# Performance work log

Measured on AMD Instinct MI355X. Metric: run time of the kernel, lower is better.

## Reference

```python
import jax, jax.numpy as jnp
import numpy as np

# priors from init_kwargs
PRIOR_PI = 0.5
PRIOR_S1 = 1.0
PRIOR_S2 = 0.0025
LOG_SQRT_2PI = 0.5 * np.log(2.0 * np.pi).astype(np.float32)


def _normal_logprob(x, sigma):
    # Normal(0, sigma).log_prob(x)
    return -0.5 * (x / sigma) ** 2 - jnp.log(sigma) - LOG_SQRT_2PI


def _mixture_logprob_sum(x, pi, sigma1, sigma2):
    # log(pi * N(x;0,s1) + (1-pi) * N(x;0,s2)).sum(), as in the torch code
    p1 = jnp.exp(_normal_logprob(x, sigma1))
    p2 = jnp.exp(_normal_logprob(x, sigma2))
    return jnp.log(pi * p1 + (1.0 - pi) * p2).sum()


def _sample(pi, rho1, rho2, eps, gum):
    # ScaleMixtureGaussian_VarPost.sample(): gumbel-max over (pi, 1-pi)
    sigma1 = jnp.log1p(jnp.exp(rho1))
    sigma2 = jnp.log1p(jnp.exp(rho2))
    x = jnp.stack((pi, 1.0 - pi), axis=-1)          # [..., 2]
    mode = jnp.argmax(x + gum, axis=-1).astype(pi.dtype)  # [...]
    return mode * sigma1 * eps + (1.0 - mode) * sigma2 * eps


def setup_inputs() -> dict:
    key = jax.random.key(0)
    ks = jax.random.split(key, 12)
    OUT, IN, B = 8192, 4096, 128
    f32 = jnp.float32
    u_w = jax.random.uniform(ks[0], (OUT, IN, 2), dtype=f32, minval=1e-6, maxval=1.0 - 1e-6)
    u_b = jax.random.uniform(ks[1], (OUT, 2), dtype=f32, minval=1e-6, maxval=1.0 - 1e-6)
    return {
        "x": jax.random.normal(ks[2], (B, IN), dtype=f32),
        "w_pi": jax.random.uniform(ks[3], (OUT, IN), dtype=f32),
        "w_rho1": 0.1 * jax.random.normal(ks[4], (OUT, IN), dtype=f32),
        "w_rho2": 0.1 * jax.random.normal(ks[5], (OUT, IN), dtype=f32),
        "b_pi": jax.random.uniform(ks[6], (OUT,), dtype=f32),
        "b_rho1": 0.1 * jax.random.normal(ks[7], (OUT,), dtype=f32),
        "b_rho2": 0.1 * jax.random.normal(ks[8], (OUT,), dtype=f32),
        "eps_w": jax.random.normal(ks[9], (OUT, IN), dtype=f32),
        "eps_b": jax.random.normal(ks[10], (OUT,), dtype=f32),
        "gum_w": -jnp.log(-jnp.log(u_w)),  # Gumbel(0,1)
        "gum_b": -jnp.log(-jnp.log(u_b)),
    }


def reference(x, w_pi, w_rho1, w_rho2, b_pi, b_rho1, b_rho2, eps_w, eps_b, gum_w, gum_b):
    weight = _sample(w_pi, w_rho1, w_rho2, eps_w, gum_w)   # [OUT, IN]
    bias = _sample(b_pi, b_rho1, b_rho2, eps_b, gum_b)     # [OUT]

    log_prior = (_mixture_logprob_sum(weight, PRIOR_PI, PRIOR_S1, PRIOR_S2)
                 + _mixture_logprob_sum(bias, PRIOR_PI, PRIOR_S1, PRIOR_S2))

    sig_w1 = jnp.log1p(jnp.exp(w_rho1))
    sig_w2 = jnp.log1p(jnp.exp(w_rho2))
    sig_b1 = jnp.log1p(jnp.exp(b_rho1))
    sig_b2 = jnp.log1p(jnp.exp(b_rho2))
    log_post = (_mixture_logprob_sum(weight, w_pi, sig_w1, sig_w2)
                + _mixture_logprob_sum(bias, b_pi, sig_b1, sig_b2))

    out = x @ weight.T + bias  # F.linear
    return out, log_prior, log_post
```

## Files before the change

### kernel.cpp

```cpp
#include <hip/hip_runtime.h>

#define OUTN 8192
#define INN  4096
#define BN   128

namespace {

typedef __attribute__((ext_vector_type(8))) short bf16x8;
typedef __attribute__((ext_vector_type(4))) float f32x4;

struct alignas(16) f4 { float v[4]; };
struct alignas(8)  h4 { short v[4]; };

constexpr float C_HLOG2PI = 0.91893853f;
constexpr float C_LN2     = 0.69314718f;

__device__ __forceinline__ short f2bf(float f) {
    unsigned u = __float_as_uint(f);
    u += 0x7fffu + ((u >> 16) & 1u);
    return (short)(u >> 16);
}

__device__ __forceinline__ float prior_lp(float w) {
    float lp1 = -0.5f * w * w - C_HLOG2PI;
    float a   = w * 400.0f;
    float lp2 = -0.5f * a * a + 5.0725261f;
    return __logf(0.5f * __expf(lp1) + 0.5f * __expf(lp2));
}
__device__ __forceinline__ float post_lp(float w, float pi_, float s1, float ls1,
                                         float s2, float ls2) {
    float u1  = __fdividef(w, s1);
    float u2  = __fdividef(w, s2);
    float lq1 = -0.5f * u1 * u1 - ls1 - C_HLOG2PI;
    float lq2 = -0.5f * u2 * u2 - ls2 - C_HLOG2PI;
    return __logf(pi_ * __expf(lq1) + (1.0f - pi_) * __expf(lq2));
}
__device__ __forceinline__ float sample_w(float pi_, float rho1, float rho2, float ep,
                                          float g0, float g1,
                                          float& s1, float& ls1, float& s2, float& ls2) {
    s1  = __logf(1.0f + __expf(rho1));
    s2  = __logf(1.0f + __expf(rho2));
    ls1 = __logf(s1);
    ls2 = __logf(s2);
    bool mode1 = ((1.0f - pi_) + g1) > (pi_ + g0);
    return (mode1 ? s1 : s2) * ep;
}

constexpr int OT = 32;
constexpr int KC = 32;
constexpr int NT = 256;
constexpr int KSTR = 40;

__global__ __launch_bounds__(256)
void prep(const float* __restrict__ x, short* __restrict__ xb,
          const float* __restrict__ b_pi, const float* __restrict__ b_rho1,
          const float* __restrict__ b_rho2, const float* __restrict__ eps_b,
          const float* __restrict__ gum_b,
          float* __restrict__ bias_vals, float* __restrict__ bpart)
{
    __shared__ float red[8];
    const int tid = threadIdx.x;
    if (blockIdx.x < 256) {
        const int i = (blockIdx.x * 256 + tid) * 8;
        f4 a = *(const f4*)&x[i];
        f4 b = *(const f4*)&x[i + 4];
        h4 o0, o1;
        #pragma unroll
        for (int j = 0; j < 4; ++j) { o0.v[j] = f2bf(a.v[j]); o1.v[j] = f2bf(b.v[j]); }
        *(h4*)&xb[i]     = o0;
        *(h4*)&xb[i + 4] = o1;
        return;
    }
    const int bb = blockIdx.x - 256;
    const int o = bb * 256 + tid;
    float pi_ = b_pi[o], rho1 = b_rho1[o], rho2 = b_rho2[o], ep = eps_b[o];
    float g0 = gum_b[2*o], g1 = gum_b[2*o + 1];
    float s1, ls1, s2, ls2;
    float w = sample_w(pi_, rho1, rho2, ep, g0, g1, s1, ls1, s2, ls2);
    bias_vals[o] = w;
    float pa = prior_lp(w);
    float qa = post_lp(w, pi_, s1, ls1, s2, ls2);
    #pragma unroll
    for (int off = 32; off; off >>= 1) {
        pa += __shfl_down(pa, off);
        qa += __shfl_down(qa, off);
    }
    const int wave = tid >> 6;
    if ((tid & 63) == 0) { red[wave] = pa; red[4 + wave] = qa; }
    __syncthreads();
    if (tid == 0) {
        bpart[2*bb    ] = red[0] + red[1] + red[2] + red[3];
        bpart[2*bb + 1] = red[4] + red[5] + red[6] + red[7];
    }
}

__global__ __launch_bounds__(NT, 6)
void bayes_main(const short* __restrict__ xb,
                const float* __restrict__ w_pi,
                const float* __restrict__ w_rho1,
                const float* __restrict__ w_rho2,
                const float* __restrict__ eps_w,
                const float* __restrict__ gum_w,
                const float* __restrict__ bias,
                float* __restrict__ out,
                float* __restrict__ pbuf,
                float* __restrict__ partials,
                int NS)
{
    __shared__ alignas(16) short Wt[2][OT][KSTR];
    __shared__ alignas(16) short Xs[2][BN][KSTR];
    __shared__ float red[8];

    const int tid   = threadIdx.x;
    const int split = blockIdx.x >> 8;
    const int tile  = blockIdx.x & 255;
    const int o0    = tile * OT;

    const int baseCh = 128 / NS;
    const int remCh  = 128 % NS;
    const int nch    = baseCh + (split < remCh ? 1 : 0);
    const int ch0    = split * baseCh + (split < remCh ? split : remCh);
    const int k0     = ch0 * KC;

    float* outp = (split == 0) ? out : pbuf + (size_t)(split - 1) * ((size_t)BN * OUTN);

    const int c = tid & 7;
    const int r = tid >> 3;

    const size_t wbase = (size_t)(o0 + r) * INN + k0;
    const f4* pi4 = (const f4*)(w_pi   + wbase) + c;
    const f4* r14 = (const f4*)(w_rho1 + wbase) + c;
    const f4* r24 = (const f4*)(w_rho2 + wbase) + c;
    const f4* ep4 = (const f4*)(eps_w  + wbase) + c;
    const f4* gm4 = (const f4*)(gum_w  + 2 * wbase) + 2 * c;

    const int xrr = tid >> 1;
    const int xcc = (tid & 1) * 16;
    const short* xsrc = xb + (size_t)xrr * INN + k0 + xcc;

    f32x4 acc00 = {0.f,0.f,0.f,0.f}, acc01 = {0.f,0.f,0.f,0.f};
    f32x4 acc10 = {0.f,0.f,0.f,0.f}, acc11 = {0.f,0.f,0.f,0.f};
    float priorAcc = 0.0f, postAcc = 0.0f;

    const int wv_  = tid >> 6;
    const int lane = tid & 63;
    const int lrow = lane & 15;
    const int lgo  = (lane >> 4) * 8;

    f4 vpi = pi4[0], vr1 = r14[0], vr2 = r24[0], vep = ep4[0];
    f4 vga = gm4[0], vgb = gm4[1];
    bf16x8 xv0 = *(const bf16x8*)(xsrc);
    bf16x8 xv1 = *(const bf16x8*)(xsrc + 8);

    #pragma unroll 1
    for (int t = 0; t < nch; ++t) {
        const int p = t & 1;
        h4 wb;
        #pragma unroll
        for (int i = 0; i < 4; ++i) {
            const f4& g = (i < 2) ? vga : vgb;
            float g0 = g.v[(i & 1) * 2], g1 = g.v[(i & 1) * 2 + 1];
            float pi_ = vpi.v[i], ep = vep.v[i];
            float s1  = __logf(1.0f + __expf(vr1.v[i]));
            float s2  = __logf(1.0f + __expf(vr2.v[i]));
            float ls1 = __logf(s1), ls2 = __logf(s2);
            bool  m1  = ((1.0f - pi_) + g1) > (pi_ + g0);
            float sm  = m1 ? s1 : s2;
            float so  = m1 ? s2 : s1;
            float lsm = m1 ? ls1 : ls2;
            float lso = m1 ? ls2 : ls1;
            float wm  = m1 ? pi_ : 1.0f - pi_;
            float w   = sm * ep;
            wb.v[i] = f2bf(w);
            float wsq = w * w;
            float dlp = 5.9914645f - 79999.5f * wsq;
            priorAcc += -0.5f * wsq + __logf(1.0f + __expf(dlp));
            float uo   = __fdividef(w, so);
            float epsq = ep * ep;
            float dlq  = 0.5f * (epsq - uo * uo) + (lsm - lso);
            postAcc += -0.5f * epsq - lsm
                       + __logf(wm + (1.0f - wm) * __expf(dlq));
        }

        const int tn = (t + 1 < nch) ? t + 1 : 0;
        vpi = pi4[8*tn]; vr1 = r14[8*tn]; vr2 = r24[8*tn]; vep = ep4[8*tn];
        vga = gm4[16*tn]; vgb = gm4[16*tn + 1];

        *(h4*)&Wt[p][r][4 * c] = wb;
        *(bf16x8*)&Xs[p][xrr][xcc]     = xv0;
        *(bf16x8*)&Xs[p][xrr][xcc + 8] = xv1;
        xv0 = *(const bf16x8*)(xsrc + 32*tn);
        xv1 = *(const bf16x8*)(xsrc + 32*tn + 8);

        asm volatile("s_waitcnt lgkmcnt(0)" ::: "memory");
        __builtin_amdgcn_s_barrier();
        asm volatile("" ::: "memory");

        bf16x8 a0 = *(const bf16x8*)&Xs[p][32 * wv_      + lrow][lgo];
        bf16x8 a1 = *(const bf16x8*)&Xs[p][32 * wv_ + 16 + lrow][lgo];
        bf16x8 b0 = *(const bf16x8*)&Wt[p][lrow     ][lgo];
        bf16x8 b1 = *(const bf16x8*)&Wt[p][16 + lrow][lgo];
        acc00 = __builtin_amdgcn_mfma_f32_16x16x32_bf16(a0, b0, acc00, 0, 0, 0);
        acc01 = __builtin_amdgcn_mfma_f32_16x16x32_bf16(a0, b1, acc01, 0, 0, 0);
        acc10 = __builtin_amdgcn_mfma_f32_16x16x32_bf16(a1, b0, acc10, 0, 0, 0);
        acc11 = __builtin_amdgcn_mfma_f32_16x16x32_bf16(a1, b1, acc11, 0, 0, 0);
    }

    {
        const float ne = (float)(4 * nch);
        priorAcc -= ne * (C_HLOG2PI + C_LN2);
        postAcc  -= ne * C_HLOG2PI;
    }

    {
        const int oc = o0 + lrow;
        const int bb = 32 * wv_ + (lane >> 4) * 4;
        const float bv0 = bias ? bias[oc]      : 0.0f;
        const float bv1 = bias ? bias[oc + 16] : 0.0f;
        #pragma unroll
        for (int j = 0; j < 4; ++j) {
            outp[(size_t)(bb      + j) * OUTN + oc     ] = acc00[j] + bv0;
            outp[(size_t)(bb      + j) * OUTN + oc + 16] = acc01[j] + bv1;
            outp[(size_t)(bb + 16 + j) * OUTN + oc     ] = acc10[j] + bv0;
            outp[(size_t)(bb + 16 + j) * OUTN + oc + 16] = acc11[j] + bv1;
        }
    }

    #pragma unroll
    for (int off = 32; off; off >>= 1) {
        priorAcc += __shfl_down(priorAcc, off);
        postAcc  += __shfl_down(postAcc, off);
    }
    if ((tid & 63) == 0) { red[wv_] = priorAcc; red[4 + wv_] = postAcc; }
    __syncthreads();
    if (tid == 0) {
        partials[2*blockIdx.x    ] = red[0] + red[1] + red[2] + red[3];
        partials[2*blockIdx.x + 1] = red[4] + red[5] + red[6] + red[7];
    }
}

__global__ __launch_bounds__(256)
void reduce_final(float* __restrict__ out, const float* __restrict__ pbuf,
                  const float* __restrict__ bias, int nsplit,
                  const float* __restrict__ partials, int cnt,
                  float* __restrict__ out_scalars)
{
    const int tid = threadIdx.x;
    const size_t i = ((size_t)blockIdx.x * 256 + tid) * 4;
    const int o = (int)(i & (OUTN - 1));
    f4 a  = *(const f4*)&out[i];
    f4 bq = *(const f4*)&bias[o];
    #pragma unroll 1
    for (int s = 0; s < nsplit - 1; ++s) {
        f4 p = *(const f4*)&pbuf[(size_t)s * ((size_t)BN * OUTN) + i];
        #pragma unroll
        for (int j = 0; j < 4; ++j) a.v[j] += p.v[j];
    }
    #pragma unroll
    for (int j = 0; j < 4; ++j) a.v[j] += bq.v[j];
    *(f4*)&out[i] = a;

    if (blockIdx.x == 0) {
        __shared__ double sp[4], sq[4];
        double p = 0.0, q = 0.0;
        for (int j = tid; j < cnt; j += 256) {
            p += (double)partials[2*j];
            q += (double)partials[2*j + 1];
        }
        #pragma unroll
        for (int off = 32; off; off >>= 1) {
            p += __shfl_down(p, off);
            q += __shfl_down(q, off);
        }
        const int wave = tid >> 6;
        if ((tid & 63) == 0) { sp[wave] = p; sq[wave] = q; }
        __syncthreads();
        if (tid == 0) {
            out_scalars[0] = (float)(sp[0] + sp[1] + sp[2] + sp[3]);
            out_scalars[1] = (float)(sq[0] + sq[1] + sq[2] + sq[3]);
        }
    }
}

__global__ __launch_bounds__(256)
void bayes_final(const float* __restrict__ partials, int cnt,
                 float* __restrict__ out_scalars)
{
    __shared__ double sp[4], sq[4];
    const int tid = threadIdx.x;
    double p = 0.0, q = 0.0;
    for (int j = tid; j < cnt; j += 256) {
        p += (double)partials[2*j];
        q += (double)partials[2*j + 1];
    }
    #pragma unroll
    for (int off = 32; off; off >>= 1) {
        p += __shfl_down(p, off);
        q += __shfl_down(q, off);
    }
    const int wave = tid >> 6;
    if ((tid & 63) == 0) { sp[wave] = p; sq[wave] = q; }
    __syncthreads();
    if (tid == 0) {
        out_scalars[0] = (float)(sp[0] + sp[1] + sp[2] + sp[3]);
        out_scalars[1] = (float)(sq[0] + sq[1] + sq[2] + sq[3]);
    }
}

}

extern "C" void kernel_launch(void* const* d_in, const int* in_sizes, int n_in,
                              void* d_out, int out_size, void* d_ws, size_t ws_size,
                              hipStream_t stream) {
    (void)in_sizes; (void)n_in; (void)out_size;
    const float* x      = (const float*)d_in[0];
    const float* w_pi   = (const float*)d_in[1];
    const float* w_rho1 = (const float*)d_in[2];
    const float* w_rho2 = (const float*)d_in[3];
    const float* b_pi   = (const float*)d_in[4];
    const float* b_rho1 = (const float*)d_in[5];
    const float* b_rho2 = (const float*)d_in[6];
    const float* eps_w  = (const float*)d_in[7];
    const float* eps_b  = (const float*)d_in[8];
    const float* gum_w  = (const float*)d_in[9];
    const float* gum_b  = (const float*)d_in[10];

    float* out = (float*)d_out;
    float* ws  = (float*)d_ws;
    float* bias_vals = ws;
    float* partials  = ws + 8192;
    short* xb        = (short*)(ws + 16384);
    float* pbuf      = ws + 540672;

    const size_t outElems = (size_t)BN * OUTN;
    int NS = 1;
    if      (ws_size >= (540672 + 5 * outElems) * sizeof(float)) NS = 6;
    else if (ws_size >= (540672 + 3 * outElems) * sizeof(float)) NS = 4;
    else if (ws_size >= (540672 + 1 * outElems) * sizeof(float)) NS = 2;

    float* bpart = partials + 2 * 256 * NS;
    const int cnt = 256 * NS + 32;

    prep<<<288, 256, 0, stream>>>(x, xb, b_pi, b_rho1, b_rho2, eps_b, gum_b,
                                  bias_vals, bpart);

    if (NS == 1) {
        bayes_main<<<256, NT, 0, stream>>>(xb, w_pi, w_rho1, w_rho2, eps_w, gum_w,
                                           bias_vals, out, pbuf, partials, 1);
        bayes_final<<<1, 256, 0, stream>>>(partials, cnt, out + outElems);
    } else {
        bayes_main<<<256 * NS, NT, 0, stream>>>(xb, w_pi, w_rho1, w_rho2, eps_w, gum_w,
                                                nullptr, out, pbuf, partials, NS);
        reduce_final<<<(int)(outElems / 4 / 256), 256, 0, stream>>>(
            out, pbuf, bias_vals, NS, partials, cnt, out + outElems);
    }
}
```

Measured before the change: 223.6 us.

## Double K chunk to 64, swizzle X shared tile, single-buffer with two barriers

Raises the per-iteration K chunk from 32 to 64, so each thread samples 8 weights and issues two MFMA k-steps per iteration, halving loop trips and barrier count. The X tile in LDS becomes a single XOR-swizzled buffer to avoid bank conflicts, and the weight tile is single-buffered with syncthreads before and after the stores. Occupancy hint drops from 6 to 5 and split-K count from 6 to 5 to match the larger tile. The trade-off is losing double buffering and the overlap of the next prefetch with LDS writes, plus higher register pressure.

```diff
diff --git a/kernel.cpp b/kernel.cpp
--- a/kernel.cpp
+++ b/kernel.cpp
@@ -47,9 +47,9 @@
 }
 
 constexpr int OT = 32;
-constexpr int KC = 32;
+constexpr int KC = 64;
 constexpr int NT = 256;
-constexpr int KSTR = 40;
+constexpr int WSTR = 72;
 
 __global__ __launch_bounds__(256)
 void prep(const float* __restrict__ x, short* __restrict__ xb,
@@ -94,7 +94,7 @@
     }
 }
 
-__global__ __launch_bounds__(NT, 6)
+__global__ __launch_bounds__(NT, 5)
 void bayes_main(const short* __restrict__ xb,
                 const float* __restrict__ w_pi,
                 const float* __restrict__ w_rho1,
@@ -107,8 +107,8 @@
                 float* __restrict__ partials,
                 int NS)
 {
-    __shared__ alignas(16) short Wt[2][OT][KSTR];
-    __shared__ alignas(16) short Xs[2][BN][KSTR];
+    __shared__ alignas(16) short Wt[OT][WSTR];
+    __shared__ alignas(16) short Xs[BN * KC];
     __shared__ float red[8];
 
     const int tid   = threadIdx.x;
@@ -116,8 +116,8 @@
     const int tile  = blockIdx.x & 255;
     const int o0    = tile * OT;
 
-    const int baseCh = 128 / NS;
-    const int remCh  = 128 % NS;
+    const int baseCh = 64 / NS;
+    const int remCh  = 64 % NS;
     const int nch    = baseCh + (split < remCh ? 1 : 0);
     const int ch0    = split * baseCh + (split < remCh ? split : remCh);
     const int k0     = ch0 * KC;
@@ -128,15 +128,16 @@
     const int r = tid >> 3;
 
     const size_t wbase = (size_t)(o0 + r) * INN + k0;
-    const f4* pi4 = (const f4*)(w_pi   + wbase) + c;
-    const f4* r14 = (const f4*)(w_rho1 + wbase) + c;
-    const f4* r24 = (const f4*)(w_rho2 + wbase) + c;
-    const f4* ep4 = (const f4*)(eps_w  + wbase) + c;
-    const f4* gm4 = (const f4*)(gum_w  + 2 * wbase) + 2 * c;
-
-    const int xrr = tid >> 1;
-    const int xcc = (tid & 1) * 16;
-    const short* xsrc = xb + (size_t)xrr * INN + k0 + xcc;
+    const f4* pi4 = (const f4*)(w_pi   + wbase) + 2 * c;
+    const f4* r14 = (const f4*)(w_rho1 + wbase) + 2 * c;
+    const f4* r24 = (const f4*)(w_rho2 + wbase) + 2 * c;
+    const f4* ep4 = (const f4*)(eps_w  + wbase) + 2 * c;
+    const f4* gm4 = (const f4*)(gum_w + 2 * wbase) + 4 * c;
+
+    const int xr   = tid >> 1;
+    const int xh   = (tid & 1) * 32;
+    const int xswz = (xr & 7) * 8;
+    const short* xsrc = xb + (size_t)xr * INN + k0 + xh;
 
     f32x4 acc00 = {0.f,0.f,0.f,0.f}, acc01 = {0.f,0.f,0.f,0.f};
     f32x4 acc10 = {0.f,0.f,0.f,0.f}, acc11 = {0.f,0.f,0.f,0.f};
@@ -146,32 +147,41 @@
     const int lane = tid & 63;
     const int lrow = lane & 15;
     const int lgo  = (lane >> 4) * 8;
-
-    f4 vpi = pi4[0], vr1 = r14[0], vr2 = r24[0], vep = ep4[0];
-    f4 vga = gm4[0], vgb = gm4[1];
+    const int rswz = (lrow & 7) * 8;
+
+    f4 p0 = pi4[0], p1 = pi4[1];
+    f4 u0 = r14[0], u1 = r14[1];
+    f4 v0 = r24[0], v1 = r24[1];
+    f4 e0 = ep4[0], e1 = ep4[1];
+    f4 g0 = gm4[0], g1 = gm4[1], g2 = gm4[2], g3 = gm4[3];
     bf16x8 xv0 = *(const bf16x8*)(xsrc);
     bf16x8 xv1 = *(const bf16x8*)(xsrc + 8);
+    bf16x8 xv2 = *(const bf16x8*)(xsrc + 16);
+    bf16x8 xv3 = *(const bf16x8*)(xsrc + 24);
 
     #pragma unroll 1
     for (int t = 0; t < nch; ++t) {
-        const int p = t & 1;
-        h4 wb;
-        #pragma unroll
-        for (int i = 0; i < 4; ++i) {
-            const f4& g = (i < 2) ? vga : vgb;
-            float g0 = g.v[(i & 1) * 2], g1 = g.v[(i & 1) * 2 + 1];
-            float pi_ = vpi.v[i], ep = vep.v[i];
-            float s1  = __logf(1.0f + __expf(vr1.v[i]));
-            float s2  = __logf(1.0f + __expf(vr2.v[i]));
+        bf16x8 wb8;
+        #pragma unroll
+        for (int j = 0; j < 8; ++j) {
+            float pi_ = ((j < 4) ? p0 : p1).v[j & 3];
+            float rh1 = ((j < 4) ? u0 : u1).v[j & 3];
+            float rh2 = ((j < 4) ? v0 : v1).v[j & 3];
+            float ep  = ((j < 4) ? e0 : e1).v[j & 3];
+            const f4& gg = (j < 2) ? g0 : (j < 4) ? g1 : (j < 6) ? g2 : g3;
+            float gg0 = gg.v[(j & 1) * 2], gg1 = gg.v[(j & 1) * 2 + 1];
+
+            float s1  = __logf(1.0f + __expf(rh1));
+            float s2  = __logf(1.0f + __expf(rh2));
             float ls1 = __logf(s1), ls2 = __logf(s2);
-            bool  m1  = ((1.0f - pi_) + g1) > (pi_ + g0);
+            bool  m1  = ((1.0f - pi_) + gg1) > (pi_ + gg0);
             float sm  = m1 ? s1 : s2;
             float so  = m1 ? s2 : s1;
             float lsm = m1 ? ls1 : ls2;
             float lso = m1 ? ls2 : ls1;
             float wm  = m1 ? pi_ : 1.0f - pi_;
             float w   = sm * ep;
-            wb.v[i] = f2bf(w);
+            wb8[j] = f2bf(w);
             float wsq = w * w;
             float dlp = 5.9914645f - 79999.5f * wsq;
             priorAcc += -0.5f * wsq + __logf(1.0f + __expf(dlp));
@@ -182,32 +192,46 @@
                        + __logf(wm + (1.0f - wm) * __expf(dlq));
         }
 
+        __syncthreads();
+        *(bf16x8*)&Wt[r][8 * c] = wb8;
+        *(bf16x8*)&Xs[xr * KC + ((xh     ) ^ xswz)] = xv0;
+        *(bf16x8*)&Xs[xr * KC + ((xh +  8) ^ xswz)] = xv1;
+        *(bf16x8*)&Xs[xr * KC + ((xh + 16) ^ xswz)] = xv2;
+        *(bf16x8*)&Xs[xr * KC + ((xh + 24) ^ xswz)] = xv3;
+        __syncthreads();
+
         const int tn = (t + 1 < nch) ? t + 1 : 0;
-        vpi = pi4[8*tn]; vr1 = r14[8*tn]; vr2 = r24[8*tn]; vep = ep4[8*tn];
-        vga = gm4[16*tn]; vgb = gm4[16*tn + 1];
-
-        *(h4*)&Wt[p][r][4 * c] = wb;
-        *(bf16x8*)&Xs[p][xrr][xcc]     = xv0;
-        *(bf16x8*)&Xs[p][xrr][xcc + 8] = xv1;
-        xv0 = *(const bf16x8*)(xsrc + 32*tn);
-        xv1 = *(const bf16x8*)(xsrc + 32*tn + 8);
-
-        asm volatile("s_waitcnt lgkmcnt(0)" ::: "memory");
-        __builtin_amdgcn_s_barrier();
-        asm volatile("" ::: "memory");
-
-        bf16x8 a0 = *(const bf16x8*)&Xs[p][32 * wv_      + lrow][lgo];
-        bf16x8 a1 = *(const bf16x8*)&Xs[p][32 * wv_ + 16 + lrow][lgo];
-        bf16x8 b0 = *(const bf16x8*)&Wt[p][lrow     ][lgo];
-        bf16x8 b1 = *(const bf16x8*)&Wt[p][16 + lrow][lgo];
-        acc00 = __builtin_amdgcn_mfma_f32_16x16x32_bf16(a0, b0, acc00, 0, 0, 0);
-        acc01 = __builtin_amdgcn_mfma_f32_16x16x32_bf16(a0, b1, acc01, 0, 0, 0);
-        acc10 = __builtin_amdgcn_mfma_f32_16x16x32_bf16(a1, b0, acc10, 0, 0, 0);
-        acc11 = __builtin_amdgcn_mfma_f32_16x16x32_bf16(a1, b1, acc11, 0, 0, 0);
+        p0 = pi4[16*tn]; p1 = pi4[16*tn + 1];
+        u0 = r14[16*tn]; u1 = r14[16*tn + 1];
+        v0 = r24[16*tn]; v1 = r24[16*tn + 1];
+        e0 = ep4[16*tn]; e1 = ep4[16*tn + 1];
+        g0 = gm4[32*tn]; g1 = gm4[32*tn + 1]; g2 = gm4[32*tn + 2]; g3 = gm4[32*tn + 3];
+        {
+            const short* xs = xsrc + 64 * tn;
+            xv0 = *(const bf16x8*)(xs);
+            xv1 = *(const bf16x8*)(xs + 8);
+            xv2 = *(const bf16x8*)(xs + 16);
+            xv3 = *(const bf16x8*)(xs + 24);
+        }
+
+        const int xrow0 = 32 * wv_ + lrow;
+        const int xrow1 = xrow0 + 16;
+        #pragma unroll
+        for (int ks = 0; ks < 2; ++ks) {
+            const int cs = ks * 32 + lgo;
+            bf16x8 a0 = *(const bf16x8*)&Xs[xrow0 * KC + (cs ^ rswz)];
+            bf16x8 a1 = *(const bf16x8*)&Xs[xrow1 * KC + (cs ^ rswz)];
+            bf16x8 b0 = *(const bf16x8*)&Wt[lrow     ][cs];
+            bf16x8 b1 = *(const bf16x8*)&Wt[16 + lrow][cs];
+            acc00 = __builtin_amdgcn_mfma_f32_16x16x32_bf16(a0, b0, acc00, 0, 0, 0);
+            acc01 = __builtin_amdgcn_mfma_f32_16x16x32_bf16(a0, b1, acc01, 0, 0, 0);
+            acc10 = __builtin_amdgcn_mfma_f32_16x16x32_bf16(a1, b0, acc10, 0, 0, 0);
+            acc11 = __builtin_amdgcn_mfma_f32_16x16x32_bf16(a1, b1, acc11, 0, 0, 0);
+        }
     }
 
     {
-        const float ne = (float)(4 * nch);
+        const float ne = (float)(8 * nch);
         priorAcc -= ne * (C_HLOG2PI + C_LN2);
         postAcc  -= ne * C_HLOG2PI;
     }
@@ -334,7 +358,7 @@
 
     const size_t outElems = (size_t)BN * OUTN;
     int NS = 1;
-    if      (ws_size >= (540672 + 5 * outElems) * sizeof(float)) NS = 6;
+    if      (ws_size >= (540672 + 4 * outElems) * sizeof(float)) NS = 5;
     else if (ws_size >= (540672 + 3 * outElems) * sizeof(float)) NS = 4;
     else if (ws_size >= (540672 + 1 * outElems) * sizeof(float)) NS = 2;
 
```

After: 214.5 us. -4.0%, faster.

## Prefetch weight parameters two chunks ahead with single LDS buffer, split K five ways

Applied to the files above, without the earlier changes.

Changes the main loop to keep two register sets of weight-parameter loads in flight, prefetching two K-chunks ahead, so global loads of pi/rho/eps/gumbel get more time to land. LDS drops from double buffering to a single buffer guarded by two barriers per iteration. The K split drops from 6 to 5 and the occupancy hint from 6 to 5 blocks. The extra barrier and the extra live registers may offset the added prefetch depth.

```diff
diff --git a/kernel.cpp b/kernel.cpp
--- a/kernel.cpp
+++ b/kernel.cpp
@@ -94,7 +94,7 @@
     }
 }
 
-__global__ __launch_bounds__(NT, 6)
+__global__ __launch_bounds__(NT, 5)
 void bayes_main(const short* __restrict__ xb,
                 const float* __restrict__ w_pi,
                 const float* __restrict__ w_rho1,
@@ -107,8 +107,8 @@
                 float* __restrict__ partials,
                 int NS)
 {
-    __shared__ alignas(16) short Wt[2][OT][KSTR];
-    __shared__ alignas(16) short Xs[2][BN][KSTR];
+    __shared__ alignas(16) short Wt[OT][KSTR];
+    __shared__ alignas(16) short Xs[BN][KSTR];
     __shared__ float red[8];
 
     const int tid   = threadIdx.x;
@@ -147,22 +147,25 @@
     const int lrow = lane & 15;
     const int lgo  = (lane >> 4) * 8;
 
-    f4 vpi = pi4[0], vr1 = r14[0], vr2 = r24[0], vep = ep4[0];
-    f4 vga = gm4[0], vgb = gm4[1];
     bf16x8 xv0 = *(const bf16x8*)(xsrc);
     bf16x8 xv1 = *(const bf16x8*)(xsrc + 8);
 
-    #pragma unroll 1
-    for (int t = 0; t < nch; ++t) {
-        const int p = t & 1;
+    f4 Ap = pi4[0], Ar1 = r14[0], Ar2 = r24[0], Ae = ep4[0];
+    f4 Aga = gm4[0], Agb = gm4[1];
+    const int t1 = (nch > 1) ? 1 : 0;
+    f4 Bp = pi4[8*t1], Br1 = r14[8*t1], Br2 = r24[8*t1], Be = ep4[8*t1];
+    f4 Bga = gm4[16*t1], Bgb = gm4[16*t1 + 1];
+
+    auto iter = [&](f4& Gp, f4& Gr1, f4& Gr2, f4& Ge, f4& Gga, f4& Ggb,
+                    int t) __attribute__((always_inline)) {
         h4 wb;
         #pragma unroll
         for (int i = 0; i < 4; ++i) {
-            const f4& g = (i < 2) ? vga : vgb;
+            const f4& g = (i < 2) ? Gga : Ggb;
             float g0 = g.v[(i & 1) * 2], g1 = g.v[(i & 1) * 2 + 1];
-            float pi_ = vpi.v[i], ep = vep.v[i];
-            float s1  = __logf(1.0f + __expf(vr1.v[i]));
-            float s2  = __logf(1.0f + __expf(vr2.v[i]));
+            float pi_ = Gp.v[i], ep = Ge.v[i];
+            float s1  = __logf(1.0f + __expf(Gr1.v[i]));
+            float s2  = __logf(1.0f + __expf(Gr2.v[i]));
             float ls1 = __logf(s1), ls2 = __logf(s2);
             bool  m1  = ((1.0f - pi_) + g1) > (pi_ + g0);
             float sm  = m1 ? s1 : s2;
@@ -182,28 +185,34 @@
                        + __logf(wm + (1.0f - wm) * __expf(dlq));
         }
 
-        const int tn = (t + 1 < nch) ? t + 1 : 0;
-        vpi = pi4[8*tn]; vr1 = r14[8*tn]; vr2 = r24[8*tn]; vep = ep4[8*tn];
-        vga = gm4[16*tn]; vgb = gm4[16*tn + 1];
-
-        *(h4*)&Wt[p][r][4 * c] = wb;
-        *(bf16x8*)&Xs[p][xrr][xcc]     = xv0;
-        *(bf16x8*)&Xs[p][xrr][xcc + 8] = xv1;
-        xv0 = *(const bf16x8*)(xsrc + 32*tn);
-        xv1 = *(const bf16x8*)(xsrc + 32*tn + 8);
-
-        asm volatile("s_waitcnt lgkmcnt(0)" ::: "memory");
-        __builtin_amdgcn_s_barrier();
-        asm volatile("" ::: "memory");
-
-        bf16x8 a0 = *(const bf16x8*)&Xs[p][32 * wv_      + lrow][lgo];
-        bf16x8 a1 = *(const bf16x8*)&Xs[p][32 * wv_ + 16 + lrow][lgo];
-        bf16x8 b0 = *(const bf16x8*)&Wt[p][lrow     ][lgo];
-        bf16x8 b1 = *(const bf16x8*)&Wt[p][16 + lrow][lgo];
+        __syncthreads();
+        *(h4*)&Wt[r][4 * c] = wb;
+        *(bf16x8*)&Xs[xrr][xcc]     = xv0;
+        *(bf16x8*)&Xs[xrr][xcc + 8] = xv1;
+        __syncthreads();
+
+        const int tg = (t + 2 < nch) ? t + 2 : nch - 1;
+        Gp = pi4[8*tg]; Gr1 = r14[8*tg]; Gr2 = r24[8*tg]; Ge = ep4[8*tg];
+        Gga = gm4[16*tg]; Ggb = gm4[16*tg + 1];
+        const int tx = (t + 1 < nch) ? t + 1 : 0;
+        xv0 = *(const bf16x8*)(xsrc + 32*tx);
+        xv1 = *(const bf16x8*)(xsrc + 32*tx + 8);
+
+        bf16x8 a0 = *(const bf16x8*)&Xs[32 * wv_      + lrow][lgo];
+        bf16x8 a1 = *(const bf16x8*)&Xs[32 * wv_ + 16 + lrow][lgo];
+        bf16x8 b0 = *(const bf16x8*)&Wt[lrow     ][lgo];
+        bf16x8 b1 = *(const bf16x8*)&Wt[16 + lrow][lgo];
         acc00 = __builtin_amdgcn_mfma_f32_16x16x32_bf16(a0, b0, acc00, 0, 0, 0);
         acc01 = __builtin_amdgcn_mfma_f32_16x16x32_bf16(a0, b1, acc01, 0, 0, 0);
         acc10 = __builtin_amdgcn_mfma_f32_16x16x32_bf16(a1, b0, acc10, 0, 0, 0);
         acc11 = __builtin_amdgcn_mfma_f32_16x16x32_bf16(a1, b1, acc11, 0, 0, 0);
+    };
+
+    #pragma unroll 1
+    for (int t = 0; t < nch; t += 2) {
+        iter(Ap, Ar1, Ar2, Ae, Aga, Agb, t);
+        if (t + 1 < nch)
+            iter(Bp, Br1, Br2, Be, Bga, Bgb, t + 1);
     }
 
     {
@@ -334,7 +343,7 @@
 
     const size_t outElems = (size_t)BN * OUTN;
     int NS = 1;
-    if      (ws_size >= (540672 + 5 * outElems) * sizeof(float)) NS = 6;
+    if      (ws_size >= (540672 + 4 * outElems) * sizeof(float)) NS = 5;
     else if (ws_size >= (540672 + 3 * outElems) * sizeof(float)) NS = 4;
     else if (ws_size >= (540672 + 1 * outElems) * sizeof(float)) NS = 2;
 
```

After: 355.5 us. +59.0%, slower.
